# Optimization experiments

Hardware: AMD Instinct MI355X
Metric: run time of the kernel (lower is better)

Reference implementation:

```python
import jax, jax.numpy as jnp
import numpy as np

HEADS = 8
DIM_HEAD = 64
SCALE = DIM_HEAD ** -0.5


def setup_inputs() -> dict:
    key = jax.random.key(0)
    k1, k2, k3 = jax.random.split(key, 3)
    x = jax.random.normal(k1, (1, 8, 16, 32, 256), dtype=jnp.float32)
    # 1x1 Conv3D kernels are pure channel matmuls; scale like glorot-ish init
    w_qkv = jax.random.normal(k2, (256, 1536), dtype=jnp.float32) * 0.02
    w_out = jax.random.normal(k3, (512, 256), dtype=jnp.float32) * 0.02
    b_out = jnp.zeros((256,), dtype=jnp.float32)
    return {"x": x, "w_qkv": w_qkv, "w_out": w_out, "b_out": b_out}


def reference(x, w_qkv, w_out, b_out):
    b, D, H, W, C = x.shape
    n = D * H * W
    # to_qkv: 1x1x1 Conv3D, no bias == channel-wise matmul
    qkv = jnp.einsum('bdhwc,cf->bdhwf', x, w_qkv)  # [b,D,H,W,3*hidden]
    q, k, v = jnp.split(qkv, 3, axis=-1)           # each [b,D,H,W,hidden]

    def to_heads(t):
        # b D H W (heads dh) -> b heads dh n
        t = t.reshape(b, n, HEADS, DIM_HEAD)
        return jnp.transpose(t, (0, 2, 3, 1))

    q = to_heads(q) * SCALE
    k = to_heads(k)
    v = to_heads(v)
    # full n x n attention, contracting over dim_head
    sim = jnp.einsum('bhdi,bhdj->bhij', q, k)      # [b,heads,n,n]
    attn = jax.nn.softmax(sim, axis=-1)
    out = jnp.einsum('bhij,bhdj->bhid', attn, v)   # [b,heads,n,dh]
    out = jnp.transpose(out, (0, 2, 1, 3)).reshape(b, D, H, W, HEADS * DIM_HEAD)
    # to_out: 1x1x1 Conv3D with bias
    return jnp.einsum('bdhwf,fc->bdhwc', out, w_out) + b_out
```

## Files before the change

### kernel.cpp

```cpp
#include <hip/hip_runtime.h>
#include <hip/hip_bf16.h>

typedef float f32x4  __attribute__((ext_vector_type(4)));
typedef float f32x16 __attribute__((ext_vector_type(16)));
typedef __bf16 bfx8  __attribute__((ext_vector_type(8)));

#define NTOK 4096
#define NHEAD 8
#define DHEAD 64
#define NSPLIT 4
#define KCHUNK (NTOK / NSPLIT)

__device__ inline f32x4 mfma16(bfx8 a, bfx8 b, f32x4 c) {
    return __builtin_amdgcn_mfma_f32_16x16x32_bf16(a, b, c, 0, 0, 0);
}
__device__ inline f32x16 mfma32(bfx8 a, bfx8 b, f32x16 c) {
    return __builtin_amdgcn_mfma_f32_32x32x16_bf16(a, b, c, 0, 0, 0);
}

__device__ __forceinline__ void gld_lds16(const __bf16* g, __bf16* lds) {
    __builtin_amdgcn_global_load_lds(
        (const __attribute__((address_space(1))) void*)g,
        (__attribute__((address_space(3))) void*)lds, 16, 0, 0);
}

__global__ __launch_bounds__(256) void cast_xw(
    const float* __restrict__ X, const float* __restrict__ Wqkv,
    const float* __restrict__ Wout,
    __bf16* __restrict__ Xb, __bf16* __restrict__ Wt, __bf16* __restrict__ Wot)
{
    __shared__ float Ws[64 * 68];
    const int bid = blockIdx.x;
    const int tid = threadIdx.x;

    if (bid < 256) {
        const float4* src = reinterpret_cast<const float4*>(X);
        int2* dst = reinterpret_cast<int2*>(Xb);
        int base = bid * 256 + tid;
#pragma unroll
        for (int i = 0; i < 4; ++i) {
            float4 v = src[base + i * 65536];
            union { __bf16 h[4]; int2 u; } o;
            o.h[0] = (__bf16)v.x; o.h[1] = (__bf16)v.y;
            o.h[2] = (__bf16)v.z; o.h[3] = (__bf16)v.w;
            dst[base + i * 65536] = o.u;
        }
    } else {
        const float* src; __bf16* dst;
        int kt, ft, srcPitch, dstPitch;
        if (bid < 352) {
            int b2 = bid - 256;
            kt = b2 / 24; ft = b2 % 24;
            src = Wqkv; srcPitch = 1536; dst = Wt; dstPitch = 256;
        } else {
            int b2 = bid - 352;
            kt = b2 >> 2; ft = b2 & 3;
            src = Wout; srcPitch = 256;  dst = Wot; dstPitch = 512;
        }
        int k0 = kt * 64, f0 = ft * 64;
#pragma unroll
        for (int rep = 0; rep < 4; ++rep) {
            int idx = rep * 256 + tid;
            int kr = idx >> 4;
            int c4 = idx & 15;
            float4 v = *reinterpret_cast<const float4*>(
                src + (size_t)(k0 + kr) * srcPitch + f0 + c4 * 4);
            *reinterpret_cast<float4*>(&Ws[kr * 68 + c4 * 4]) = v;
        }
        __syncthreads();
        int fr = tid & 63;
        int kg = tid >> 6;
        union { __bf16 h[8]; int4 u; } o0, o1;
#pragma unroll
        for (int j = 0; j < 8; ++j) o0.h[j] = (__bf16)Ws[(kg * 16 + j) * 68 + fr];
#pragma unroll
        for (int j = 0; j < 8; ++j) o1.h[j] = (__bf16)Ws[(kg * 16 + 8 + j) * 68 + fr];
        int4* d = reinterpret_cast<int4*>(dst + (size_t)(f0 + fr) * dstPitch + k0 + kg * 16);
        d[0] = o0.u; d[1] = o1.u;
    }
}

__global__ __launch_bounds__(256) void gemm_qkv_b(
    const __bf16* __restrict__ Xb, const __bf16* __restrict__ Wt,
    __bf16* __restrict__ Q, __bf16* __restrict__ Kb, __bf16* __restrict__ Vt)
{
    __shared__ __bf16 As[128 * 64];
    __shared__ __bf16 Bs[128 * 64];
    const int tid  = threadIdx.x;
    const int lane = tid & 63;
    const int wv   = tid >> 6;
    const int wr   = wv >> 1, wc = wv & 1;
    const int m0 = blockIdx.y * 128;
    const int n0 = blockIdx.x * 128;
    const int l15 = lane & 15, l4 = lane >> 4;

    f32x4 zero = {0.f, 0.f, 0.f, 0.f};
    f32x4 acc[4][4];
#pragma unroll
    for (int i = 0; i < 4; ++i)
#pragma unroll
        for (int j = 0; j < 4; ++j) acc[i][j] = zero;

    const int srow8 = lane >> 3;
    const int sslot = lane & 7;

    for (int k0 = 0; k0 < 256; k0 += 64) {
#pragma unroll
        for (int j = 0; j < 4; ++j) {
            int rbase = j * 32 + wv * 8;
            int row   = rbase + srow8;
            int slot  = sslot ^ (row & 7);
            gld_lds16(Xb + (size_t)(m0 + row) * 256 + k0 + slot * 8, &As[rbase * 64]);
            gld_lds16(Wt + (size_t)(n0 + row) * 256 + k0 + slot * 8, &Bs[rbase * 64]);
        }
        __syncthreads();

#pragma unroll
        for (int s = 0; s < 2; ++s) {
            bfx8 af[4], bf_[4];
#pragma unroll
            for (int m = 0; m < 4; ++m) {
                int row = wr * 64 + m * 16 + l15;
                af[m] = *reinterpret_cast<const bfx8*>(
                    reinterpret_cast<const char*>(As) + row * 128 +
                    (((s * 4 + l4) * 16) ^ ((row & 7) << 4)));
            }
#pragma unroll
            for (int n = 0; n < 4; ++n) {
                int row = wc * 64 + n * 16 + l15;
                bf_[n] = *reinterpret_cast<const bfx8*>(
                    reinterpret_cast<const char*>(Bs) + row * 128 +
                    (((s * 4 + l4) * 16) ^ ((row & 7) << 4)));
            }
#pragma unroll
            for (int m = 0; m < 4; ++m)
#pragma unroll
                for (int n = 0; n < 4; ++n)
                    acc[m][n] = mfma16(af[m], bf_[n], acc[m][n]);
        }
        __syncthreads();
    }

    const float QSCALE = 0.125f * 1.44269504088896f;
#pragma unroll
    for (int m = 0; m < 4; ++m)
#pragma unroll
        for (int n = 0; n < 4; ++n) {
            int rowb = m0 + wr * 64 + m * 16 + l4 * 4;
            int f    = n0 + wc * 64 + n * 16 + l15;
            if (f < 512) {
#pragma unroll
                for (int r = 0; r < 4; ++r)
                    Q[(size_t)(f >> 6) * (NTOK * DHEAD) + (size_t)(rowb + r) * DHEAD + (f & 63)] =
                        (__bf16)(acc[m][n][r] * QSCALE);
            } else if (f < 1024) {
                int g = f - 512;
#pragma unroll
                for (int r = 0; r < 4; ++r)
                    Kb[(size_t)(g >> 6) * (NTOK * DHEAD) + (size_t)(rowb + r) * DHEAD + (g & 63)] =
                        (__bf16)acc[m][n][r];
            } else {
                int g = f - 1024;
                union { __bf16 h[4]; int2 u; } o;
                o.h[0] = (__bf16)acc[m][n][0]; o.h[1] = (__bf16)acc[m][n][1];
                o.h[2] = (__bf16)acc[m][n][2]; o.h[3] = (__bf16)acc[m][n][3];
                *reinterpret_cast<int2*>(
                    Vt + (size_t)(g >> 6) * (DHEAD * NTOK) + (size_t)(g & 63) * NTOK + rowb) = o.u;
            }
        }
}

__global__ __launch_bounds__(512, 4) void attn_fwd(
    const __bf16* __restrict__ Q, const __bf16* __restrict__ Kb,
    const __bf16* __restrict__ Vt,
    __bf16* __restrict__ Opart, float* __restrict__ Lsum)
{
    const int tid  = threadIdx.x;
    const int lane = tid & 63;
    const int wv   = tid >> 6;
    const int bid = blockIdx.x;
    const int h  = bid & 7;
    const int t2 = bid >> 3;
    const int sp = t2 & (NSPLIT - 1);
    const int qb = t2 >> 2;
    const int l31 = lane & 31;
    const int hi  = lane >> 5;

    const __bf16* Qh = Q  + (size_t)h * NTOK * DHEAD;
    const __bf16* Kh = Kb + (size_t)h * NTOK * DHEAD;
    const __bf16* Vh = Vt + (size_t)h * DHEAD * NTOK;

    __shared__ __bf16 Ks[2][64 * 64];
    __shared__ __bf16 Vs[2][64 * 64];

    const int srow  = tid >> 3;
    const int scol8 = (tid & 7) ^ (srow & 7);

    const int qrow = qb * 256 + wv * 32 + l31;
    bfx8 qf[4];
#pragma unroll
    for (int s = 0; s < 4; ++s)
        qf[s] = *reinterpret_cast<const bfx8*>(
            Qh + (size_t)qrow * DHEAD + s * 16 + hi * 8);

    f32x16 o0, o1;
#pragma unroll
    for (int r = 0; r < 16; ++r) { o0[r] = 0.f; o1[r] = 0.f; }
    float l_l = 0.f;

    const int jbeg = sp * KCHUNK, jend = jbeg + KCHUNK;
    const int ksw = (l31 & 7) << 4;

    auto stage = [&](int bf, int j0) {
        gld_lds16(Kh + (size_t)(j0 + srow) * DHEAD + scol8 * 8, &Ks[bf][wv * 8 * 64]);
        gld_lds16(Vh + (size_t)srow * NTOK + j0 + scol8 * 8,    &Vs[bf][wv * 8 * 64]);
    };

    stage(0, jbeg);
    __syncthreads();

    int buf = 0;
    for (int j0 = jbeg; j0 < jend; j0 += 64) {
        if (j0 + 64 < jend) stage(buf ^ 1, j0 + 64);

        const char* Kt  = reinterpret_cast<const char*>(&Ks[buf][0]);
        const char* Vtc = reinterpret_cast<const char*>(&Vs[buf][0]);

#pragma unroll
        for (int kb = 0; kb < 2; ++kb) {
            const char* Kr = Kt + (kb * 32 + l31) * 128;
            f32x16 sa;
#pragma unroll
            for (int r = 0; r < 16; ++r) sa[r] = 0.f;
            __builtin_amdgcn_s_setprio(1);
#pragma unroll
            for (int s = 0; s < 4; ++s) {
                bfx8 kf = *reinterpret_cast<const bfx8*>(Kr + (((s * 2 + hi) * 16) ^ ksw));
                sa = mfma32(kf, qf[s], sa);
            }
            __builtin_amdgcn_s_setprio(0);

            float p0  = __builtin_amdgcn_exp2f(sa[0]);
            float p1  = __builtin_amdgcn_exp2f(sa[1]);
            float p2  = __builtin_amdgcn_exp2f(sa[2]);
            float p3  = __builtin_amdgcn_exp2f(sa[3]);
            float p4  = __builtin_amdgcn_exp2f(sa[4]);
            float p5  = __builtin_amdgcn_exp2f(sa[5]);
            float p6  = __builtin_amdgcn_exp2f(sa[6]);
            float p7  = __builtin_amdgcn_exp2f(sa[7]);
            float p8  = __builtin_amdgcn_exp2f(sa[8]);
            float p9  = __builtin_amdgcn_exp2f(sa[9]);
            float p10 = __builtin_amdgcn_exp2f(sa[10]);
            float p11 = __builtin_amdgcn_exp2f(sa[11]);
            float p12 = __builtin_amdgcn_exp2f(sa[12]);
            float p13 = __builtin_amdgcn_exp2f(sa[13]);
            float p14 = __builtin_amdgcn_exp2f(sa[14]);
            float p15 = __builtin_amdgcn_exp2f(sa[15]);
            float ps = ((p0 + p1) + (p2 + p3)) + ((p4 + p5) + (p6 + p7))
                     + ((p8 + p9) + (p10 + p11)) + ((p12 + p13) + (p14 + p15));
            ps += __shfl_xor(ps, 32, 64);
            l_l += ps;

            unsigned int a0, a1, a2, a3, a4, a5, a6, a7;
            asm("v_cvt_pk_bf16_f32 %0, %1, %2" : "=v"(a0) : "v"(p0),  "v"(p1));
            asm("v_cvt_pk_bf16_f32 %0, %1, %2" : "=v"(a1) : "v"(p2),  "v"(p3));
            asm("v_cvt_pk_bf16_f32 %0, %1, %2" : "=v"(a2) : "v"(p4),  "v"(p5));
            asm("v_cvt_pk_bf16_f32 %0, %1, %2" : "=v"(a3) : "v"(p6),  "v"(p7));
            asm("v_cvt_pk_bf16_f32 %0, %1, %2" : "=v"(a4) : "v"(p8),  "v"(p9));
            asm("v_cvt_pk_bf16_f32 %0, %1, %2" : "=v"(a5) : "v"(p10), "v"(p11));
            asm("v_cvt_pk_bf16_f32 %0, %1, %2" : "=v"(a6) : "v"(p12), "v"(p13));
            asm("v_cvt_pk_bf16_f32 %0, %1, %2" : "=v"(a7) : "v"(p14), "v"(p15));
            asm("v_permlane32_swap_b32 %0, %1" : "+v"(a0), "+v"(a2));
            asm("v_permlane32_swap_b32 %0, %1" : "+v"(a1), "+v"(a3));
            asm("v_permlane32_swap_b32 %0, %1" : "+v"(a4), "+v"(a6));
            asm("v_permlane32_swap_b32 %0, %1" : "+v"(a5), "+v"(a7));
            union { unsigned int u[4]; bfx8 v; } f1, f2;
            f1.u[0] = a0; f1.u[1] = a1; f1.u[2] = a2; f1.u[3] = a3;
            f2.u[0] = a4; f2.u[1] = a5; f2.u[2] = a6; f2.u[3] = a7;

            __builtin_amdgcn_s_setprio(1);
            {
                int cb0 = (kb * 64 + hi * 16) ^ ksw;
                bfx8 vf00 = *reinterpret_cast<const bfx8*>(Vtc + l31 * 128 + cb0);
                o0 = mfma32(f1.v, vf00, o0);
                bfx8 vf01 = *reinterpret_cast<const bfx8*>(Vtc + (32 + l31) * 128 + cb0);
                o1 = mfma32(f1.v, vf01, o1);
                int cb1 = (kb * 64 + 32 + hi * 16) ^ ksw;
                bfx8 vf10 = *reinterpret_cast<const bfx8*>(Vtc + l31 * 128 + cb1);
                o0 = mfma32(f2.v, vf10, o0);
                bfx8 vf11 = *reinterpret_cast<const bfx8*>(Vtc + (32 + l31) * 128 + cb1);
                o1 = mfma32(f2.v, vf11, o1);
            }
            __builtin_amdgcn_s_setprio(0);
        }

        __syncthreads();
        buf ^= 1;
    }

#pragma unroll
    for (int r = 0; r < 16; ++r) {
        int q = (r & 3) + 8 * (r >> 2) + 4 * hi;
        size_t row = (size_t)(qb * 256 + wv * 32 + q);
        __bf16* dst = Opart + ((size_t)sp * NTOK + row) * 512 + h * 64 + l31;
        dst[0]  = (__bf16)o0[r];
        dst[32] = (__bf16)o1[r];
    }
    if (hi == 0) {
        Lsum[((size_t)sp * NHEAD + h) * NTOK + qrow] = l_l;
    }
}

__global__ __launch_bounds__(256) void attn_combine(
    const __bf16* __restrict__ Opart, const float* __restrict__ Lsum,
    __bf16* __restrict__ O)
{
    int idx = blockIdx.x * 256 + threadIdx.x;
    int row = idx >> 7;
    int c4  = (idx & 127) * 4;
    int h   = c4 >> 6;

    float denom = 0.f;
    float4 acc = make_float4(0.f, 0.f, 0.f, 0.f);
#pragma unroll
    for (int s = 0; s < NSPLIT; ++s) {
        denom += Lsum[((size_t)s * NHEAD + h) * NTOK + row];
        union { int2 u; __bf16 h[4]; } v;
        v.u = *reinterpret_cast<const int2*>(
            Opart + ((size_t)s * NTOK + row) * 512 + c4);
        acc.x += (float)v.h[0]; acc.y += (float)v.h[1];
        acc.z += (float)v.h[2]; acc.w += (float)v.h[3];
    }
    float inv = 1.f / denom;
    __bf16* op = O + (size_t)row * 512 + c4;
    op[0] = (__bf16)(acc.x * inv); op[1] = (__bf16)(acc.y * inv);
    op[2] = (__bf16)(acc.z * inv); op[3] = (__bf16)(acc.w * inv);
}

__global__ __launch_bounds__(256) void gemm_out_b(
    const __bf16* __restrict__ O, const __bf16* __restrict__ Wot,
    const float* __restrict__ bias, float* __restrict__ out)
{
    __shared__ __bf16 As[64 * 64];
    __shared__ __bf16 Bs[64 * 64];
    const int tid  = threadIdx.x;
    const int lane = tid & 63;
    const int wv   = tid >> 6;
    const int wr   = wv >> 1, wc = wv & 1;
    const int m0 = blockIdx.y * 64;
    const int n0 = blockIdx.x * 64;
    const int l15 = lane & 15, l4 = lane >> 4;

    f32x4 zero = {0.f, 0.f, 0.f, 0.f};
    f32x4 acc[2][2];
#pragma unroll
    for (int i = 0; i < 2; ++i)
#pragma unroll
        for (int j = 0; j < 2; ++j) acc[i][j] = zero;

    const int srow8 = lane >> 3;
    const int sslot = lane & 7;

    for (int k0 = 0; k0 < 512; k0 += 64) {
#pragma unroll
        for (int j = 0; j < 2; ++j) {
            int rbase = j * 32 + wv * 8;
            int row   = rbase + srow8;
            int slot  = sslot ^ (row & 7);
            gld_lds16(O   + (size_t)(m0 + row) * 512 + k0 + slot * 8, &As[rbase * 64]);
            gld_lds16(Wot + (size_t)(n0 + row) * 512 + k0 + slot * 8, &Bs[rbase * 64]);
        }
        __syncthreads();

#pragma unroll
        for (int s = 0; s < 2; ++s) {
            bfx8 af[2], bf_[2];
#pragma unroll
            for (int m = 0; m < 2; ++m) {
                int row = wr * 32 + m * 16 + l15;
                af[m] = *reinterpret_cast<const bfx8*>(
                    reinterpret_cast<const char*>(As) + row * 128 +
                    (((s * 4 + l4) * 16) ^ ((row & 7) << 4)));
            }
#pragma unroll
            for (int n = 0; n < 2; ++n) {
                int row = wc * 32 + n * 16 + l15;
                bf_[n] = *reinterpret_cast<const bfx8*>(
                    reinterpret_cast<const char*>(Bs) + row * 128 +
                    (((s * 4 + l4) * 16) ^ ((row & 7) << 4)));
            }
#pragma unroll
            for (int m = 0; m < 2; ++m)
#pragma unroll
                for (int n = 0; n < 2; ++n)
                    acc[m][n] = mfma16(af[m], bf_[n], acc[m][n]);
        }
        __syncthreads();
    }

#pragma unroll
    for (int m = 0; m < 2; ++m)
#pragma unroll
        for (int n = 0; n < 2; ++n) {
            int col = n0 + wc * 32 + n * 16 + l15;
            float b = bias[col];
#pragma unroll
            for (int r = 0; r < 4; ++r) {
                int row = m0 + wr * 32 + m * 16 + l4 * 4 + r;
                out[(size_t)row * 256 + col] = acc[m][n][r] + b;
            }
        }
}

extern "C" void kernel_launch(void* const* d_in, const int* in_sizes, int n_in,
                              void* d_out, int out_size, void* d_ws, size_t ws_size,
                              hipStream_t stream) {
    const float* x     = (const float*)d_in[0];
    const float* w_qkv = (const float*)d_in[1];
    const float* w_out = (const float*)d_in[2];
    const float* b_out = (const float*)d_in[3];
    float* out = (float*)d_out;

    __bf16* Q  = (__bf16*)d_ws;
    __bf16* K  = Q  + (size_t)NHEAD * NTOK * DHEAD;
    __bf16* Vt = K  + (size_t)NHEAD * NTOK * DHEAD;
    __bf16* O  = Vt + (size_t)NHEAD * NTOK * DHEAD;
    __bf16* Opart = O + (size_t)NTOK * 512;
    float* Lsum = (float*)(Opart + (size_t)NSPLIT * NTOK * 512);
    __bf16* Xb = (__bf16*)(Lsum + (size_t)NSPLIT * NHEAD * NTOK);
    __bf16* Wt = Xb + (size_t)NTOK * 256;
    __bf16* Wot = Wt + (size_t)1536 * 256;

    cast_xw     <<<dim3(384), 256, 0, stream>>>(x, w_qkv, w_out, Xb, Wt, Wot);
    gemm_qkv_b  <<<dim3(12, 32), 256, 0, stream>>>(Xb, Wt, Q, K, Vt);
    attn_fwd    <<<dim3((NTOK / 256) * NSPLIT * NHEAD), 512, 0, stream>>>(Q, K, Vt, Opart, Lsum);
    attn_combine<<<dim3(NTOK * 128 / 256), 256, 0, stream>>>(Opart, Lsum, O);
    gemm_out_b  <<<dim3(256 / 64, NTOK / 64), 256, 0, stream>>>(O, Wot, b_out, out);
}
```

Before: 72.46 us.

## Fuse split-K attention combine into output GEMM and restructure softmax/PV loop

Removes the separate attn_combine kernel and the O buffer: the output GEMM now reads the four partial outputs and row sums directly, normalizes them and writes the A tile into shared memory. The attention inner loop computes both 32-key QK tiles up front before softmax and PV, and moves the cross-half row-sum shuffle out of the loop to run once at the end. This saves one launch and a global round-trip of O. In exchange, the GEMM reads the partial outputs redundantly for each of its four column blocks.

```diff
diff --git a/kernel.cpp b/kernel.cpp
--- a/kernel.cpp
+++ b/kernel.cpp
@@ -169,6 +169,57 @@
             }
         }
 }
+
+#define SM_PACK(SA, F1, F2)                                                   \
+    {                                                                         \
+        float e0  = __builtin_amdgcn_exp2f(SA[0]);                            \
+        float e1  = __builtin_amdgcn_exp2f(SA[1]);                            \
+        float e2  = __builtin_amdgcn_exp2f(SA[2]);                            \
+        float e3  = __builtin_amdgcn_exp2f(SA[3]);                            \
+        float e4  = __builtin_amdgcn_exp2f(SA[4]);                            \
+        float e5  = __builtin_amdgcn_exp2f(SA[5]);                            \
+        float e6  = __builtin_amdgcn_exp2f(SA[6]);                            \
+        float e7  = __builtin_amdgcn_exp2f(SA[7]);                            \
+        float e8  = __builtin_amdgcn_exp2f(SA[8]);                            \
+        float e9  = __builtin_amdgcn_exp2f(SA[9]);                            \
+        float e10 = __builtin_amdgcn_exp2f(SA[10]);                           \
+        float e11 = __builtin_amdgcn_exp2f(SA[11]);                           \
+        float e12 = __builtin_amdgcn_exp2f(SA[12]);                           \
+        float e13 = __builtin_amdgcn_exp2f(SA[13]);                           \
+        float e14 = __builtin_amdgcn_exp2f(SA[14]);                           \
+        float e15 = __builtin_amdgcn_exp2f(SA[15]);                           \
+        l0 += (((e0 + e1) + (e2 + e3)) + ((e4 + e5) + (e6 + e7)))             \
+            + (((e8 + e9) + (e10 + e11)) + ((e12 + e13) + (e14 + e15)));      \
+        unsigned int b0, b1, b2, b3, b4, b5, b6, b7;                          \
+        asm("v_cvt_pk_bf16_f32 %0, %1, %2" : "=v"(b0) : "v"(e0),  "v"(e1));   \
+        asm("v_cvt_pk_bf16_f32 %0, %1, %2" : "=v"(b1) : "v"(e2),  "v"(e3));   \
+        asm("v_cvt_pk_bf16_f32 %0, %1, %2" : "=v"(b2) : "v"(e4),  "v"(e5));   \
+        asm("v_cvt_pk_bf16_f32 %0, %1, %2" : "=v"(b3) : "v"(e6),  "v"(e7));   \
+        asm("v_cvt_pk_bf16_f32 %0, %1, %2" : "=v"(b4) : "v"(e8),  "v"(e9));   \
+        asm("v_cvt_pk_bf16_f32 %0, %1, %2" : "=v"(b5) : "v"(e10), "v"(e11));  \
+        asm("v_cvt_pk_bf16_f32 %0, %1, %2" : "=v"(b6) : "v"(e12), "v"(e13));  \
+        asm("v_cvt_pk_bf16_f32 %0, %1, %2" : "=v"(b7) : "v"(e14), "v"(e15));  \
+        asm("v_permlane32_swap_b32 %0, %1" : "+v"(b0), "+v"(b2));             \
+        asm("v_permlane32_swap_b32 %0, %1" : "+v"(b1), "+v"(b3));             \
+        asm("v_permlane32_swap_b32 %0, %1" : "+v"(b4), "+v"(b6));             \
+        asm("v_permlane32_swap_b32 %0, %1" : "+v"(b5), "+v"(b7));             \
+        F1.u[0] = b0; F1.u[1] = b1; F1.u[2] = b2; F1.u[3] = b3;               \
+        F2.u[0] = b4; F2.u[1] = b5; F2.u[2] = b6; F2.u[3] = b7;               \
+    }
+
+#define PV_ACC(KB, F1, F2)                                                        \
+    {                                                                             \
+        int cb0 = ((KB) * 64 + hi * 16) ^ ksw;                                    \
+        bfx8 vf00 = *reinterpret_cast<const bfx8*>(Vtc + l31 * 128 + cb0);        \
+        o0 = mfma32(F1.v, vf00, o0);                                              \
+        bfx8 vf01 = *reinterpret_cast<const bfx8*>(Vtc + (32 + l31) * 128 + cb0); \
+        o1 = mfma32(F1.v, vf01, o1);                                              \
+        int cb1 = ((KB) * 64 + 32 + hi * 16) ^ ksw;                               \
+        bfx8 vf10 = *reinterpret_cast<const bfx8*>(Vtc + l31 * 128 + cb1);        \
+        o0 = mfma32(F2.v, vf10, o0);                                              \
+        bfx8 vf11 = *reinterpret_cast<const bfx8*>(Vtc + (32 + l31) * 128 + cb1); \
+        o1 = mfma32(F2.v, vf11, o1);                                              \
+    }
 
 __global__ __launch_bounds__(512, 4) void attn_fwd(
     const __bf16* __restrict__ Q, const __bf16* __restrict__ Kb,
@@ -206,7 +257,7 @@
     f32x16 o0, o1;
 #pragma unroll
     for (int r = 0; r < 16; ++r) { o0[r] = 0.f; o1[r] = 0.f; }
-    float l_l = 0.f;
+    float l0 = 0.f;
 
     const int jbeg = sp * KCHUNK, jend = jbeg + KCHUNK;
     const int ksw = (l31 & 7) << 4;
@@ -226,77 +277,39 @@
         const char* Kt  = reinterpret_cast<const char*>(&Ks[buf][0]);
         const char* Vtc = reinterpret_cast<const char*>(&Vs[buf][0]);
 
-#pragma unroll
-        for (int kb = 0; kb < 2; ++kb) {
-            const char* Kr = Kt + (kb * 32 + l31) * 128;
-            f32x16 sa;
-#pragma unroll
-            for (int r = 0; r < 16; ++r) sa[r] = 0.f;
-            __builtin_amdgcn_s_setprio(1);
-#pragma unroll
-            for (int s = 0; s < 4; ++s) {
-                bfx8 kf = *reinterpret_cast<const bfx8*>(Kr + (((s * 2 + hi) * 16) ^ ksw));
-                sa = mfma32(kf, qf[s], sa);
-            }
-            __builtin_amdgcn_s_setprio(0);
-
-            float p0  = __builtin_amdgcn_exp2f(sa[0]);
-            float p1  = __builtin_amdgcn_exp2f(sa[1]);
-            float p2  = __builtin_amdgcn_exp2f(sa[2]);
-            float p3  = __builtin_amdgcn_exp2f(sa[3]);
-            float p4  = __builtin_amdgcn_exp2f(sa[4]);
-            float p5  = __builtin_amdgcn_exp2f(sa[5]);
-            float p6  = __builtin_amdgcn_exp2f(sa[6]);
-            float p7  = __builtin_amdgcn_exp2f(sa[7]);
-            float p8  = __builtin_amdgcn_exp2f(sa[8]);
-            float p9  = __builtin_amdgcn_exp2f(sa[9]);
-            float p10 = __builtin_amdgcn_exp2f(sa[10]);
-            float p11 = __builtin_amdgcn_exp2f(sa[11]);
-            float p12 = __builtin_amdgcn_exp2f(sa[12]);
-            float p13 = __builtin_amdgcn_exp2f(sa[13]);
-            float p14 = __builtin_amdgcn_exp2f(sa[14]);
-            float p15 = __builtin_amdgcn_exp2f(sa[15]);
-            float ps = ((p0 + p1) + (p2 + p3)) + ((p4 + p5) + (p6 + p7))
-                     + ((p8 + p9) + (p10 + p11)) + ((p12 + p13) + (p14 + p15));
-            ps += __shfl_xor(ps, 32, 64);
-            l_l += ps;
-
-            unsigned int a0, a1, a2, a3, a4, a5, a6, a7;
-            asm("v_cvt_pk_bf16_f32 %0, %1, %2" : "=v"(a0) : "v"(p0),  "v"(p1));
-            asm("v_cvt_pk_bf16_f32 %0, %1, %2" : "=v"(a1) : "v"(p2),  "v"(p3));
-            asm("v_cvt_pk_bf16_f32 %0, %1, %2" : "=v"(a2) : "v"(p4),  "v"(p5));
-            asm("v_cvt_pk_bf16_f32 %0, %1, %2" : "=v"(a3) : "v"(p6),  "v"(p7));
-            asm("v_cvt_pk_bf16_f32 %0, %1, %2" : "=v"(a4) : "v"(p8),  "v"(p9));
-            asm("v_cvt_pk_bf16_f32 %0, %1, %2" : "=v"(a5) : "v"(p10), "v"(p11));
-            asm("v_cvt_pk_bf16_f32 %0, %1, %2" : "=v"(a6) : "v"(p12), "v"(p13));
-            asm("v_cvt_pk_bf16_f32 %0, %1, %2" : "=v"(a7) : "v"(p14), "v"(p15));
-            asm("v_permlane32_swap_b32 %0, %1" : "+v"(a0), "+v"(a2));
-            asm("v_permlane32_swap_b32 %0, %1" : "+v"(a1), "+v"(a3));
-            asm("v_permlane32_swap_b32 %0, %1" : "+v"(a4), "+v"(a6));
-            asm("v_permlane32_swap_b32 %0, %1" : "+v"(a5), "+v"(a7));
-            union { unsigned int u[4]; bfx8 v; } f1, f2;
-            f1.u[0] = a0; f1.u[1] = a1; f1.u[2] = a2; f1.u[3] = a3;
-            f2.u[0] = a4; f2.u[1] = a5; f2.u[2] = a6; f2.u[3] = a7;
-
-            __builtin_amdgcn_s_setprio(1);
-            {
-                int cb0 = (kb * 64 + hi * 16) ^ ksw;
-                bfx8 vf00 = *reinterpret_cast<const bfx8*>(Vtc + l31 * 128 + cb0);
-                o0 = mfma32(f1.v, vf00, o0);
-                bfx8 vf01 = *reinterpret_cast<const bfx8*>(Vtc + (32 + l31) * 128 + cb0);
-                o1 = mfma32(f1.v, vf01, o1);
-                int cb1 = (kb * 64 + 32 + hi * 16) ^ ksw;
-                bfx8 vf10 = *reinterpret_cast<const bfx8*>(Vtc + l31 * 128 + cb1);
-                o0 = mfma32(f2.v, vf10, o0);
-                bfx8 vf11 = *reinterpret_cast<const bfx8*>(Vtc + (32 + l31) * 128 + cb1);
-                o1 = mfma32(f2.v, vf11, o1);
-            }
-            __builtin_amdgcn_s_setprio(0);
-        }
+        const char* Kr0 = Kt + l31 * 128;
+        const char* Kr1 = Kt + (32 + l31) * 128;
+        f32x16 sa0, sa1;
+#pragma unroll
+        for (int r = 0; r < 16; ++r) { sa0[r] = 0.f; sa1[r] = 0.f; }
+        __builtin_amdgcn_s_setprio(1);
+#pragma unroll
+        for (int s = 0; s < 4; ++s) {
+            bfx8 kf0 = *reinterpret_cast<const bfx8*>(Kr0 + (((s * 2 + hi) * 16) ^ ksw));
+            sa0 = mfma32(kf0, qf[s], sa0);
+        }
+#pragma unroll
+        for (int s = 0; s < 4; ++s) {
+            bfx8 kf1 = *reinterpret_cast<const bfx8*>(Kr1 + (((s * 2 + hi) * 16) ^ ksw));
+            sa1 = mfma32(kf1, qf[s], sa1);
+        }
+        __builtin_amdgcn_s_setprio(0);
+
+        union { unsigned int u[4]; bfx8 v; } f10, f20, f11, f21;
+        SM_PACK(sa0, f10, f20);
+        __builtin_amdgcn_s_setprio(1);
+        PV_ACC(0, f10, f20);
+        __builtin_amdgcn_s_setprio(0);
+        SM_PACK(sa1, f11, f21);
+        __builtin_amdgcn_s_setprio(1);
+        PV_ACC(1, f11, f21);
+        __builtin_amdgcn_s_setprio(0);
 
         __syncthreads();
         buf ^= 1;
     }
+
+    float l_l = l0 + __shfl_xor(l0, 32, 64);
 
 #pragma unroll
     for (int r = 0; r < 16; ++r) {
@@ -311,35 +324,10 @@
     }
 }
 
-__global__ __launch_bounds__(256) void attn_combine(
+__global__ __launch_bounds__(256) void gemm_out_f(
     const __bf16* __restrict__ Opart, const float* __restrict__ Lsum,
-    __bf16* __restrict__ O)
-{
-    int idx = blockIdx.x * 256 + threadIdx.x;
-    int row = idx >> 7;
-    int c4  = (idx & 127) * 4;
-    int h   = c4 >> 6;
-
-    float denom = 0.f;
-    float4 acc = make_float4(0.f, 0.f, 0.f, 0.f);
-#pragma unroll
-    for (int s = 0; s < NSPLIT; ++s) {
-        denom += Lsum[((size_t)s * NHEAD + h) * NTOK + row];
-        union { int2 u; __bf16 h[4]; } v;
-        v.u = *reinterpret_cast<const int2*>(
-            Opart + ((size_t)s * NTOK + row) * 512 + c4);
-        acc.x += (float)v.h[0]; acc.y += (float)v.h[1];
-        acc.z += (float)v.h[2]; acc.w += (float)v.h[3];
-    }
-    float inv = 1.f / denom;
-    __bf16* op = O + (size_t)row * 512 + c4;
-    op[0] = (__bf16)(acc.x * inv); op[1] = (__bf16)(acc.y * inv);
-    op[2] = (__bf16)(acc.z * inv); op[3] = (__bf16)(acc.w * inv);
-}
-
-__global__ __launch_bounds__(256) void gemm_out_b(
-    const __bf16* __restrict__ O, const __bf16* __restrict__ Wot,
-    const float* __restrict__ bias, float* __restrict__ out)
+    const __bf16* __restrict__ Wot, const float* __restrict__ bias,
+    float* __restrict__ out)
 {
     __shared__ __bf16 As[64 * 64];
     __shared__ __bf16 Bs[64 * 64];
@@ -360,15 +348,49 @@
 
     const int srow8 = lane >> 3;
     const int sslot = lane & 7;
+    const int arow  = tid >> 2;
+    const int aseg  = tid & 3;
 
     for (int k0 = 0; k0 < 512; k0 += 64) {
+        const int h = k0 >> 6;
 #pragma unroll
         for (int j = 0; j < 2; ++j) {
             int rbase = j * 32 + wv * 8;
             int row   = rbase + srow8;
             int slot  = sslot ^ (row & 7);
-            gld_lds16(O   + (size_t)(m0 + row) * 512 + k0 + slot * 8, &As[rbase * 64]);
             gld_lds16(Wot + (size_t)(n0 + row) * 512 + k0 + slot * 8, &Bs[rbase * 64]);
+        }
+        {
+            int grow = m0 + arow;
+            float d = Lsum[(size_t)(0 * NHEAD + h) * NTOK + grow]
+                    + Lsum[(size_t)(1 * NHEAD + h) * NTOK + grow]
+                    + Lsum[(size_t)(2 * NHEAD + h) * NTOK + grow]
+                    + Lsum[(size_t)(3 * NHEAD + h) * NTOK + grow];
+            float inv = 1.f / d;
+            float fa[16];
+#pragma unroll
+            for (int j = 0; j < 16; ++j) fa[j] = 0.f;
+#pragma unroll
+            for (int s = 0; s < NSPLIT; ++s) {
+                union { int4 u; __bf16 hh[8]; } v0, v1;
+                const __bf16* src = Opart + ((size_t)s * NTOK + grow) * 512 + k0 + aseg * 16;
+                v0.u = *reinterpret_cast<const int4*>(src);
+                v1.u = *reinterpret_cast<const int4*>(src + 8);
+#pragma unroll
+                for (int j = 0; j < 8; ++j) fa[j]     += (float)v0.hh[j];
+#pragma unroll
+                for (int j = 0; j < 8; ++j) fa[8 + j] += (float)v1.hh[j];
+            }
+            union { __bf16 hh[8]; int4 u; } w0, w1;
+#pragma unroll
+            for (int j = 0; j < 8; ++j) w0.hh[j] = (__bf16)(fa[j] * inv);
+#pragma unroll
+            for (int j = 0; j < 8; ++j) w1.hh[j] = (__bf16)(fa[8 + j] * inv);
+            char* ab = reinterpret_cast<char*>(As) + arow * 128;
+            int slot0 = (aseg * 2)     ^ (arow & 7);
+            int slot1 = (aseg * 2 + 1) ^ (arow & 7);
+            *reinterpret_cast<int4*>(ab + slot0 * 16) = w0.u;
+            *reinterpret_cast<int4*>(ab + slot1 * 16) = w1.u;
         }
         __syncthreads();
 
@@ -424,16 +446,14 @@
     __bf16* Q  = (__bf16*)d_ws;
     __bf16* K  = Q  + (size_t)NHEAD * NTOK * DHEAD;
     __bf16* Vt = K  + (size_t)NHEAD * NTOK * DHEAD;
-    __bf16* O  = Vt + (size_t)NHEAD * NTOK * DHEAD;
-    __bf16* Opart = O + (size_t)NTOK * 512;
+    __bf16* Opart = Vt + (size_t)NHEAD * NTOK * DHEAD;
     float* Lsum = (float*)(Opart + (size_t)NSPLIT * NTOK * 512);
     __bf16* Xb = (__bf16*)(Lsum + (size_t)NSPLIT * NHEAD * NTOK);
     __bf16* Wt = Xb + (size_t)NTOK * 256;
     __bf16* Wot = Wt + (size_t)1536 * 256;
 
-    cast_xw     <<<dim3(384), 256, 0, stream>>>(x, w_qkv, w_out, Xb, Wt, Wot);
-    gemm_qkv_b  <<<dim3(12, 32), 256, 0, stream>>>(Xb, Wt, Q, K, Vt);
-    attn_fwd    <<<dim3((NTOK / 256) * NSPLIT * NHEAD), 512, 0, stream>>>(Q, K, Vt, Opart, Lsum);
-    attn_combine<<<dim3(NTOK * 128 / 256), 256, 0, stream>>>(Opart, Lsum, O);
-    gemm_out_b  <<<dim3(256 / 64, NTOK / 64), 256, 0, stream>>>(O, Wot, b_out, out);
-}
+    cast_xw   <<<dim3(384), 256, 0, stream>>>(x, w_qkv, w_out, Xb, Wt, Wot);
+    gemm_qkv_b<<<dim3(12, 32), 256, 0, stream>>>(Xb, Wt, Q, K, Vt);
+    attn_fwd  <<<dim3((NTOK / 256) * NSPLIT * NHEAD), 512, 0, stream>>>(Q, K, Vt, Opart, Lsum);
+    gemm_out_f<<<dim3(256 / 64, NTOK / 64), 256, 0, stream>>>(Opart, Lsum, Wot, b_out, out);
+}
```

Result: slower. 75.26 us (+3.9%).
